# Optimization experiments

Hardware: AMD Instinct MI355X
Metric: run time of the kernel (lower is better)

## Reference

```python
import jax, jax.numpy as jnp
import numpy as np

EMB_DIM = 1024
HEAD = 16
HEAD_DIM = EMB_DIM // HEAD


def setup_inputs() -> dict:
    key = jax.random.key(0)
    ks = jax.random.split(key, 6)
    s = 1.0 / np.sqrt(EMB_DIM)
    return {
        "z": jax.random.normal(ks[0], (4, 2048, EMB_DIM), dtype=jnp.float32),
        "w_q": jax.random.normal(ks[1], (EMB_DIM, EMB_DIM), dtype=jnp.float32) * s,
        "w_k": jax.random.normal(ks[2], (EMB_DIM, EMB_DIM), dtype=jnp.float32) * s,
        "w_v": jax.random.normal(ks[3], (EMB_DIM, EMB_DIM), dtype=jnp.float32) * s,
        "w_o": jax.random.normal(ks[4], (EMB_DIM, EMB_DIM), dtype=jnp.float32) * s,
        "b_o": jax.random.normal(ks[5], (EMB_DIM,), dtype=jnp.float32) * 0.01,
    }


def reference(z, w_q, w_k, w_v, w_o, b_o):
    B, N, D = z.shape
    # QKV projections (nn.Linear: x @ W.T; here weights stored as (D_in, D_out))
    q = (z @ w_q).reshape(B, N, HEAD, HEAD_DIM).transpose(0, 2, 1, 3)  # bhnd
    k = (z @ w_k).reshape(B, N, HEAD, HEAD_DIM).transpose(0, 2, 1, 3)
    v = (z @ w_v).reshape(B, N, HEAD, HEAD_DIM).transpose(0, 2, 1, 3)
    scale = 1.0 / np.sqrt(HEAD_DIM).astype(np.float32)
    dots = jnp.einsum("bhnd,bhmd->bhnm", q, k) * scale
    attn = jax.nn.softmax(dots, axis=-1)
    out = jnp.einsum("bhnm,bhmd->bhnd", attn, v)
    out = out.transpose(0, 2, 1, 3).reshape(B, N, D)
    return out @ w_o + b_o
```

## Files before the change

### kernel.cpp

```cpp
#include <hip/hip_runtime.h>
#include <hip/hip_bf16.h>
#include <stdint.h>

typedef unsigned short u16;
typedef __attribute__((ext_vector_type(8))) short bf16x8;
typedef __attribute__((ext_vector_type(4))) float f32x4;
typedef __attribute__((ext_vector_type(16))) float f32x16;

static __device__ inline u16 f2bf(float f) {
  union { float f; uint32_t u; } v; v.f = f;
  uint32_t u = v.u;
  u += 0x7fffu + ((u >> 16) & 1);
  return (u16)(u >> 16);
}

static __device__ inline float fast_exp2(float x) {
#if __has_builtin(__builtin_amdgcn_exp2f)
  return __builtin_amdgcn_exp2f(x);
#else
  return __expf(x * 0.6931471805599453f);
#endif
}

static __device__ inline uint32_t pack_bf16(float lo, float hi) {
#if __has_builtin(__builtin_amdgcn_cvt_pk_bf16_f32)
  typedef __attribute__((ext_vector_type(2))) __bf16 bf16x2_t;
  bf16x2_t r = __builtin_amdgcn_cvt_pk_bf16_f32(lo, hi);
  union { bf16x2_t v; uint32_t u; } c; c.v = r;
  return c.u;
#else
  union { float f; uint32_t u; } a, b;
  a.f = lo; b.f = hi;
  uint32_t ua = a.u + 0x8000u;
  uint32_t ub = b.u + 0x8000u;
  return __builtin_amdgcn_perm(ub, ua, 0x07060302u);
#endif
}

static __device__ __forceinline__ void plswap(uint32_t a, uint32_t b,
                                              uint32_t& x, uint32_t& y) {
#if __has_builtin(__builtin_amdgcn_permlane32_swap)
  auto r = __builtin_amdgcn_permlane32_swap(a, b, false, false);
  x = (uint32_t)r[0]; y = (uint32_t)r[1];
#else
  int h = (threadIdx.x & 63) >> 5;
  uint32_t pa = (uint32_t)__shfl_xor((int)a, 32, 64);
  uint32_t pb = (uint32_t)__shfl_xor((int)b, 32, 64);
  x = h ? pb : a;
  y = h ? b : pa;
#endif
}

static __device__ __forceinline__ void load_lds_128(const u16* g, u16* l) {
  __builtin_amdgcn_global_load_lds((const __attribute__((address_space(1))) void*)g,
                                   (__attribute__((address_space(3))) void*)l,
                                   16, 0, 0);
}

__global__ __launch_bounds__(256) void cast_bf16_kernel(const float* __restrict__ src,
                                                        u16* __restrict__ dst, int n4) {
  int i = blockIdx.x * 256 + threadIdx.x;
  if (i < n4) {
    float4 v = reinterpret_cast<const float4*>(src)[i];
    uint2 o;
    o.x = pack_bf16(v.x, v.y);
    o.y = pack_bf16(v.z, v.w);
    reinterpret_cast<uint2*>(dst)[i] = o;
  }
}

__global__ __launch_bounds__(256) void wtrans_kernel(const float* __restrict__ wq,
                                                     const float* __restrict__ wk,
                                                     const float* __restrict__ wv,
                                                     const float* __restrict__ wo,
                                                     u16* __restrict__ bqkv,
                                                     u16* __restrict__ wot) {
  int z = blockIdx.z;
  const float* src = (z == 0) ? wq : (z == 1) ? wk : (z == 2) ? wv : wo;
  u16* dst = (z < 3) ? (bqkv + (size_t)z * 1024 * 1024) : wot;
  __shared__ float tile[32][33];
  int c0 = blockIdx.x * 32, r0 = blockIdx.y * 32;
  int tx = threadIdx.x, ty = threadIdx.y;
#pragma unroll
  for (int i = 0; i < 32; i += 8)
    tile[ty + i][tx] = src[(size_t)(r0 + ty + i) * 1024 + c0 + tx];
  __syncthreads();
#pragma unroll
  for (int i = 0; i < 32; i += 8)
    dst[(size_t)(c0 + ty + i) * 1024 + r0 + tx] = f2bf(tile[tx][ty + i]);
}

template <int MODE>
__global__ __launch_bounds__(256) void gemm_bt_kernel(
    const u16* __restrict__ A, const u16* __restrict__ Bt,
    u16* __restrict__ outQ, u16* __restrict__ outK, u16* __restrict__ outVt,
    float* __restrict__ outC, const float* __restrict__ bias) {
  const int Kd = 1024;
  const int n0 = blockIdx.x * 128;
  const int m0 = blockIdx.y * 128;
  __shared__ __align__(16) u16 Asm[128 * 32];
  __shared__ __align__(16) u16 Bsm[128 * 32];
  const int tid = threadIdx.x;
  const int wave = tid >> 6, lane = tid & 63;
  const int quad = lane >> 4, l15 = lane & 15;
  const int wm = (wave >> 1) * 64, wn = (wave & 1) * 64;

  const int c0 = wave * 128 + lane;
  const int c1 = c0 + 64;
  const int r0 = c0 >> 2, p0 = (c0 & 3) * 8;
  const int r1 = c1 >> 2, p1 = (c1 & 3) * 8;

  const u16* Ab = A + (size_t)m0 * Kd;
  const u16* Bb = Bt + (size_t)n0 * Kd;

  f32x4 acc[4][4] = {};

  for (int k0 = 0; k0 < Kd; k0 += 32) {
    __syncthreads();
    load_lds_128(Ab + (size_t)r0 * Kd + k0 + p0, Asm + c0 * 8);
    load_lds_128(Ab + (size_t)r1 * Kd + k0 + p1, Asm + c1 * 8);
    load_lds_128(Bb + (size_t)r0 * Kd + k0 + p0, Bsm + c0 * 8);
    load_lds_128(Bb + (size_t)r1 * Kd + k0 + p1, Bsm + c1 * 8);
    __syncthreads();
    bf16x8 af[4], bf[4];
#pragma unroll
    for (int i = 0; i < 4; i++)
      af[i] = *reinterpret_cast<const bf16x8*>(Asm + (wm + i * 16 + l15) * 32 + quad * 8);
#pragma unroll
    for (int i = 0; i < 4; i++)
      bf[i] = *reinterpret_cast<const bf16x8*>(Bsm + (wn + i * 16 + l15) * 32 + quad * 8);
#pragma unroll
    for (int mi = 0; mi < 4; mi++)
#pragma unroll
      for (int ni = 0; ni < 4; ni++)
        acc[mi][ni] = __builtin_amdgcn_mfma_f32_16x16x32_bf16(af[mi], bf[ni], acc[mi][ni], 0, 0, 0);
  }

  if (MODE == 0) {
    const int which = (n0 + wn) >> 10;
#pragma unroll
    for (int mi = 0; mi < 4; mi++)
#pragma unroll
      for (int ni = 0; ni < 4; ni++) {
        int n = n0 + wn + ni * 16 + l15;
        int hn = n & 1023;
        int h = hn >> 6, dim = hn & 63;
        if (which == 2) {
          int m = m0 + wm + mi * 16 + quad * 4;
          int b = m >> 11, tok = m & 2047;
          uint2 pk;
          pk.x = pack_bf16(acc[mi][ni][0], acc[mi][ni][1]);
          pk.y = pack_bf16(acc[mi][ni][2], acc[mi][ni][3]);
          *reinterpret_cast<uint2*>(outVt + ((size_t)(b * 16 + h) * 64 + dim) * 2048 + tok) = pk;
        } else {
          u16* dst = (which == 0) ? outQ : outK;
          float qscale = (which == 0) ? 0.1803368801111204f : 1.0f;
#pragma unroll
          for (int r = 0; r < 4; r++) {
            int m = m0 + wm + mi * 16 + quad * 4 + r;
            int b = m >> 11, tok = m & 2047;
            dst[(((size_t)(b * 16 + h)) * 2048 + tok) * 64 + dim] = f2bf(acc[mi][ni][r] * qscale);
          }
        }
      }
  } else {
#pragma unroll
    for (int mi = 0; mi < 4; mi++)
#pragma unroll
      for (int ni = 0; ni < 4; ni++) {
        int n = n0 + wn + ni * 16 + l15;
        float bv = bias[n];
#pragma unroll
        for (int r = 0; r < 4; r++) {
          int m = m0 + wm + mi * 16 + quad * 4 + r;
          outC[(size_t)m * 1024 + n] = acc[mi][ni][r] + bv;
        }
      }
  }
}

__global__ __launch_bounds__(256, 2) void attn_kernel(const u16* __restrict__ Q,
                                                      const u16* __restrict__ K,
                                                      const u16* __restrict__ Vt,
                                                      u16* __restrict__ Oout) {
  const int bh = blockIdx.x;
  const int q0 = blockIdx.y * 256;
  const int tid = threadIdx.x;
  const int wave = tid >> 6, lane = tid & 63;
  const int l31 = lane & 31, h = lane >> 5;
  const int e = l31 & 7;

  __shared__ __align__(16) u16 Kb2[2][4096];
  __shared__ __align__(16) u16 Vb2[2][4096];

  const u16* Qg = Q + ((size_t)bh * 2048 + q0 + wave * 64) * 64;
  const u16* Kg = K + (size_t)bh * 2048 * 64;
  const u16* Vg = Vt + (size_t)bh * 64 * 2048;

  bf16x8 qf[2][4];
#pragma unroll
  for (int j = 0; j < 2; j++)
#pragma unroll
    for (int dc = 0; dc < 4; dc++)
      qf[j][dc] = *reinterpret_cast<const bf16x8*>(
          Qg + (size_t)(j * 32 + l31) * 64 + dc * 16 + h * 8);

  const int s0 = tid, s1 = tid + 256;
  const int sr0 = s0 >> 3, sg0 = ((s0 & 7) ^ (sr0 & 7)) * 8;
  const int sr1 = s1 >> 3, sg1 = ((s1 & 7) ^ (sr1 & 7)) * 8;

  load_lds_128(Kg + (size_t)sr0 * 64 + sg0, &Kb2[0][s0 * 8]);
  load_lds_128(Kg + (size_t)sr1 * 64 + sg1, &Kb2[0][s1 * 8]);
  load_lds_128(Vg + (size_t)sr0 * 2048 + sg0, &Vb2[0][s0 * 8]);
  load_lds_128(Vg + (size_t)sr1 * 2048 + sg1, &Vb2[0][s1 * 8]);
  __syncthreads();

  float ls[2][2] = {};
  f32x16 oacc[2][2] = {};
  int cur = 0;

  for (int kt = 0; kt < 2048; kt += 64) {
    const u16* uK = &Kb2[cur][0];
    const u16* uV = &Vb2[cur][0];

    bf16x8 kfr[2][4], vfr[2][2][2];
#pragma unroll
    for (int kb = 0; kb < 2; kb++)
#pragma unroll
      for (int dc = 0; dc < 4; dc++)
        kfr[kb][dc] = *reinterpret_cast<const bf16x8*>(
            uK + (kb * 32 + l31) * 64 + (((2 * dc + h) ^ e) * 8));
#pragma unroll
    for (int dt = 0; dt < 2; dt++)
#pragma unroll
      for (int kb = 0; kb < 2; kb++)
#pragma unroll
        for (int kc = 0; kc < 2; kc++)
          vfr[dt][kb][kc] = *reinterpret_cast<const bf16x8*>(
              uV + (dt * 32 + l31) * 64 + (((4 * kb + 2 * kc + h) ^ e) * 8));

    if (kt + 64 < 2048) {
      const int nb = cur ^ 1;
      load_lds_128(Kg + (size_t)(kt + 64 + sr0) * 64 + sg0, &Kb2[nb][s0 * 8]);
      load_lds_128(Kg + (size_t)(kt + 64 + sr1) * 64 + sg1, &Kb2[nb][s1 * 8]);
      load_lds_128(Vg + (size_t)sr0 * 2048 + kt + 64 + sg0, &Vb2[nb][s0 * 8]);
      load_lds_128(Vg + (size_t)sr1 * 2048 + kt + 64 + sg1, &Vb2[nb][s1 * 8]);
    }

#pragma unroll
    for (int kb = 0; kb < 2; kb++)
#pragma unroll
      for (int j = 0; j < 2; j++) {
        f32x16 s = {};
#pragma unroll
        for (int dc = 0; dc < 4; dc++)
          s = __builtin_amdgcn_mfma_f32_32x32x16_bf16(kfr[kb][dc], qf[j][dc], s, 0, 0, 0);
        float p[16];
#pragma unroll
        for (int i = 0; i < 16; i++) p[i] = fast_exp2(s[i]);
#pragma unroll
        for (int i = 0; i < 16; i += 2) { ls[j][0] += p[i]; ls[j][1] += p[i + 1]; }
        uint32_t pk[4][2];
#pragma unroll
        for (int rq = 0; rq < 4; rq++) {
          pk[rq][0] = pack_bf16(p[rq * 4 + 0], p[rq * 4 + 1]);
          pk[rq][1] = pack_bf16(p[rq * 4 + 2], p[rq * 4 + 3]);
        }
        uint4 b0, b1;
        plswap(pk[0][0], pk[1][0], b0.x, b0.z);
        plswap(pk[0][1], pk[1][1], b0.y, b0.w);
        plswap(pk[2][0], pk[3][0], b1.x, b1.z);
        plswap(pk[2][1], pk[3][1], b1.y, b1.w);
        union { uint4 u; bf16x8 v; } bf0, bf1;
        bf0.u = b0; bf1.u = b1;
#pragma unroll
        for (int dt = 0; dt < 2; dt++) {
          oacc[j][dt] = __builtin_amdgcn_mfma_f32_32x32x16_bf16(vfr[dt][kb][0], bf0.v, oacc[j][dt], 0, 0, 0);
          oacc[j][dt] = __builtin_amdgcn_mfma_f32_32x32x16_bf16(vfr[dt][kb][1], bf1.v, oacc[j][dt], 0, 0, 0);
        }
      }

    __syncthreads();
    cur ^= 1;
  }

  const int b = bh >> 4, hd = bh & 15;
  u16* dst = Oout + (size_t)b * 2048 * 1024 + (size_t)hd * 64;
#pragma unroll
  for (int j = 0; j < 2; j++) {
    float lsum = ls[j][0] + ls[j][1];
    lsum += __shfl_xor(lsum, 32, 64);
    float inv = __builtin_amdgcn_rcpf(lsum);
    const size_t qrow = (size_t)(q0 + wave * 64 + j * 32 + l31) * 1024;
#pragma unroll
    for (int dt = 0; dt < 2; dt++)
#pragma unroll
      for (int rq = 0; rq < 4; rq++) {
        uint2 o;
        o.x = pack_bf16(oacc[j][dt][rq * 4 + 0] * inv, oacc[j][dt][rq * 4 + 1] * inv);
        o.y = pack_bf16(oacc[j][dt][rq * 4 + 2] * inv, oacc[j][dt][rq * 4 + 3] * inv);
        *reinterpret_cast<uint2*>(dst + qrow + dt * 32 + rq * 8 + h * 4) = o;
      }
  }
}

extern "C" void kernel_launch(void* const* d_in, const int* in_sizes, int n_in,
                              void* d_out, int out_size, void* d_ws, size_t ws_size,
                              hipStream_t stream) {
  (void)in_sizes; (void)n_in; (void)out_size; (void)ws_size;
  const float* z  = (const float*)d_in[0];
  const float* wq = (const float*)d_in[1];
  const float* wk = (const float*)d_in[2];
  const float* wv = (const float*)d_in[3];
  const float* wo = (const float*)d_in[4];
  const float* bo = (const float*)d_in[5];
  float* out = (float*)d_out;

  char* ws = (char*)d_ws;
  u16* zb   = (u16*)(ws);
  u16* bqkv = (u16*)(ws + (16ull << 20));
  u16* wot  = (u16*)(ws + (22ull << 20));
  u16* Qb   = (u16*)(ws + (24ull << 20));
  u16* Kb   = (u16*)(ws + (40ull << 20));
  u16* Vtb  = (u16*)(ws + (56ull << 20));
  u16* Ob   = zb;

  cast_bf16_kernel<<<8192, 256, 0, stream>>>(z, zb, 2097152);
  wtrans_kernel<<<dim3(32, 32, 4), dim3(32, 8), 0, stream>>>(wq, wk, wv, wo, bqkv, wot);
  gemm_bt_kernel<0><<<dim3(24, 64), 256, 0, stream>>>(zb, bqkv, Qb, Kb, Vtb, nullptr, nullptr);
  attn_kernel<<<dim3(64, 8), 256, 0, stream>>>(Qb, Kb, Vtb, Ob);
  gemm_bt_kernel<1><<<dim3(8, 64), 256, 0, stream>>>(Ob, wot, nullptr, nullptr, nullptr, out, bo);
}
```

Before: 281.8 us.

## Replace QKV projection GEMM with 256x256-tile, 8-wave pipelined kernel

Adds a new QKV projection GEMM that uses 256x256 output tiles with 512 threads. It double-buffers LDS with direct global-to-LDS loads, interleaves staging of the next K-slice with MFMA phases separated by barriers, and raises wave priority during the MFMA phases. Workgroup IDs are remapped in an XCD-aware way to improve L2 locality. Larger tiles raise arithmetic intensity and reduce the number of blocks, at the cost of heavy LDS use (128 KB), register pressure, and fewer blocks to balance across CUs.

```diff
diff --git a/kernel.cpp b/kernel.cpp
--- a/kernel.cpp
+++ b/kernel.cpp
@@ -179,6 +179,136 @@
   }
 }
 
+__global__ __launch_bounds__(512, 2) void gemm256_kernel(
+    const u16* __restrict__ A, const u16* __restrict__ Bt,
+    u16* __restrict__ outQ, u16* __restrict__ outK, u16* __restrict__ outVt) {
+  const int tid = threadIdx.x;
+  const int lane = tid & 63;
+  const int wave = tid >> 6;
+  const int quad = lane >> 4, l15 = lane & 15;
+  const int e15 = l15 & 7;
+  const int wm = wave >> 2;
+  const int wn = wave & 3;
+
+  unsigned lin = blockIdx.y * gridDim.x + blockIdx.x;
+  unsigned nwg = gridDim.x * gridDim.y;
+  lin = (lin & 7u) * (nwg >> 3) + (lin >> 3);
+  const int bx = lin % gridDim.x, by = lin / gridDim.x;
+  const int n0 = bx * 256, m0 = by * 256;
+
+  __shared__ __align__(16) u16 AsmL[2][16384];
+  __shared__ __align__(16) u16 BsmL[2][16384];
+  u16* const As_[2] = {&AsmL[0][0], &AsmL[1][0]};
+  u16* const Bs_[2] = {&BsmL[0][0], &BsmL[1][0]};
+
+  const u16* Abase = A + (size_t)m0 * 1024;
+  const u16* Bbase = Bt + (size_t)n0 * 1024;
+
+  const int awoff = wm * 8192;
+  const int bwoff = (wn >> 1) * 8192 + (wn & 1) * 4096;
+
+  f32x4 acc[8][4] = {};
+  bf16x8 af[4][2], bfr[4][2];
+
+#define STG_HALF(ldsp, gp)                                                      \
+  {                                                                             \
+    const int cs0 = tid, cs1 = tid + 512;                                       \
+    const int r0_ = cs0 >> 3, g0_ = (((cs0 & 7) ^ (r0_ & 7)) << 3);             \
+    const int r1_ = cs1 >> 3, g1_ = (((cs1 & 7) ^ (r1_ & 7)) << 3);             \
+    load_lds_128((gp) + (size_t)r0_ * 1024 + g0_, (ldsp) + cs0 * 8);            \
+    load_lds_128((gp) + (size_t)r1_ * 1024 + g1_, (ldsp) + cs1 * 8);            \
+  }
+
+#define PHB() do { asm volatile("" ::: "memory"); __builtin_amdgcn_s_barrier(); \
+                   asm volatile("" ::: "memory"); } while (0)
+#define LGKM0() asm volatile("s_waitcnt lgkmcnt(0)" ::: "memory")
+#define VMC8()  asm volatile("s_waitcnt vmcnt(8)" ::: "memory")
+
+#define RD_A(mb, B)                                                             \
+  _Pragma("unroll") for (int x = 0; x < 4; x++)                                 \
+  _Pragma("unroll") for (int kk = 0; kk < 2; kk++)                              \
+    af[x][kk] = *reinterpret_cast<const bf16x8*>(                               \
+        As_[B] + awoff + (((mb) + x) * 16 + l15) * 64 + (((quad + kk * 4) ^ e15) << 3));
+
+#define RD_B(nb, B)                                                             \
+  _Pragma("unroll") for (int x = 0; x < 2; x++)                                 \
+  _Pragma("unroll") for (int kk = 0; kk < 2; kk++)                              \
+    bfr[(nb) + x][kk] = *reinterpret_cast<const bf16x8*>(                       \
+        Bs_[B] + bwoff + (((nb) + x) * 16 + l15) * 64 + (((quad + kk * 4) ^ e15) << 3));
+
+#define MM(mb, nb)                                                              \
+  _Pragma("unroll") for (int kk = 0; kk < 2; kk++)                              \
+  _Pragma("unroll") for (int x = 0; x < 4; x++)                                 \
+  _Pragma("unroll") for (int y = 0; y < 2; y++)                                 \
+    acc[(mb) + x][(nb) + y] = __builtin_amdgcn_mfma_f32_16x16x32_bf16(          \
+        af[x][kk], bfr[(nb) + y][kk], acc[(mb) + x][(nb) + y], 0, 0, 0);
+
+#define TILE4(B, KS)                                                            \
+  RD_A(0, B); RD_B(0, B);                                                       \
+  PHB(); LGKM0(); __builtin_amdgcn_s_setprio(1); MM(0, 0);                      \
+  __builtin_amdgcn_s_setprio(0); PHB();                                         \
+  RD_B(2, B);                                                                   \
+  PHB(); LGKM0(); __builtin_amdgcn_s_setprio(1); MM(0, 2);                      \
+  __builtin_amdgcn_s_setprio(0); PHB();                                         \
+  RD_A(4, B);                                                                   \
+  STG_HALF(Bs_[B], Bbase + (KS)); STG_HALF(Bs_[B] + 8192, Bbase + 128 * 1024 + (KS)); \
+  PHB(); LGKM0(); __builtin_amdgcn_s_setprio(1); MM(4, 0);                      \
+  __builtin_amdgcn_s_setprio(0); PHB();                                         \
+  STG_HALF(As_[B], Abase + (KS)); STG_HALF(As_[B] + 8192, Abase + 128 * 1024 + (KS)); \
+  PHB(); __builtin_amdgcn_s_setprio(1); MM(4, 2);                               \
+  __builtin_amdgcn_s_setprio(0); VMC8(); PHB();
+
+  STG_HALF(As_[0], Abase);      STG_HALF(As_[0] + 8192, Abase + 128 * 1024);
+  STG_HALF(Bs_[0], Bbase);      STG_HALF(Bs_[0] + 8192, Bbase + 128 * 1024);
+  STG_HALF(As_[1], Abase + 64); STG_HALF(As_[1] + 8192, Abase + 128 * 1024 + 64);
+  STG_HALF(Bs_[1], Bbase + 64); STG_HALF(Bs_[1] + 8192, Bbase + 128 * 1024 + 64);
+  VMC8(); PHB();
+
+#pragma unroll 1
+  for (int it = 0; it < 8; ++it) {
+    int t2 = it * 2 + 2; if (t2 > 15) t2 = 15;
+    int t3 = it * 2 + 3; if (t3 > 15) t3 = 15;
+    const int k2 = t2 * 64, k3 = t3 * 64;
+    TILE4(0, k2);
+    TILE4(1, k3);
+  }
+
+  const int which = (n0 + wn * 64) >> 10;
+#pragma unroll
+  for (int mi = 0; mi < 8; mi++)
+#pragma unroll
+    for (int ni = 0; ni < 4; ni++) {
+      int n = n0 + wn * 64 + ni * 16 + l15;
+      int hn = n & 1023;
+      int hh = hn >> 6, dim = hn & 63;
+      if (which == 2) {
+        int m = m0 + wm * 128 + mi * 16 + quad * 4;
+        int b = m >> 11, tok = m & 2047;
+        uint2 pk;
+        pk.x = pack_bf16(acc[mi][ni][0], acc[mi][ni][1]);
+        pk.y = pack_bf16(acc[mi][ni][2], acc[mi][ni][3]);
+        *reinterpret_cast<uint2*>(outVt + ((size_t)(b * 16 + hh) * 64 + dim) * 2048 + tok) = pk;
+      } else {
+        u16* dst = (which == 0) ? outQ : outK;
+        float qscale = (which == 0) ? 0.1803368801111204f : 1.0f;
+#pragma unroll
+        for (int r = 0; r < 4; r++) {
+          int m = m0 + wm * 128 + mi * 16 + quad * 4 + r;
+          int b = m >> 11, tok = m & 2047;
+          dst[(((size_t)(b * 16 + hh)) * 2048 + tok) * 64 + dim] = f2bf(acc[mi][ni][r] * qscale);
+        }
+      }
+    }
+#undef STG_HALF
+#undef PHB
+#undef LGKM0
+#undef VMC8
+#undef RD_A
+#undef RD_B
+#undef MM
+#undef TILE4
+}
+
 __global__ __launch_bounds__(256, 2) void attn_kernel(const u16* __restrict__ Q,
                                                       const u16* __restrict__ K,
                                                       const u16* __restrict__ Vt,
@@ -327,7 +457,7 @@
 
   cast_bf16_kernel<<<8192, 256, 0, stream>>>(z, zb, 2097152);
   wtrans_kernel<<<dim3(32, 32, 4), dim3(32, 8), 0, stream>>>(wq, wk, wv, wo, bqkv, wot);
-  gemm_bt_kernel<0><<<dim3(24, 64), 256, 0, stream>>>(zb, bqkv, Qb, Kb, Vtb, nullptr, nullptr);
+  gemm256_kernel<<<dim3(12, 32), 512, 0, stream>>>(zb, bqkv, Qb, Kb, Vtb);
   attn_kernel<<<dim3(64, 8), 256, 0, stream>>>(Qb, Kb, Vtb, Ob);
   gemm_bt_kernel<1><<<dim3(8, 64), 256, 0, stream>>>(Ob, wot, nullptr, nullptr, nullptr, out, bo);
 }
```

New measurement: 281.6 us. Within noise of the previous version (-0.1%).
